# Performance work log

Measured on AMD Instinct MI355X. Metric: run time of the kernel, lower is better.

Reference implementation:

```python
import jax, jax.numpy as jnp
import numpy as np

D_MODEL = 1024
D_HEAD = 128


def setup_inputs() -> dict:
    key = jax.random.key(0)
    kx, kq, kk, kv, ko = jax.random.split(key, 5)
    x = jax.random.normal(kx, (4, 2048, D_MODEL), dtype=jnp.float32)
    # xavier-uniform-ish init scale
    s_in = (6.0 / (D_MODEL + D_HEAD)) ** 0.5
    wq = jax.random.uniform(kq, (D_MODEL, D_HEAD), minval=-s_in, maxval=s_in, dtype=jnp.float32)
    wk = jax.random.uniform(kk, (D_MODEL, D_HEAD), minval=-s_in, maxval=s_in, dtype=jnp.float32)
    wv = jax.random.uniform(kv, (D_MODEL, D_HEAD), minval=-s_in, maxval=s_in, dtype=jnp.float32)
    wo = jax.random.uniform(ko, (D_HEAD, D_MODEL), minval=-s_in, maxval=s_in, dtype=jnp.float32)
    return {"x": x, "wq": wq, "wk": wk, "wv": wv, "wo": wo}


def reference(x, wq, wk, wv, wo):
    # x: [b, s, d_model]
    s = x.shape[1]
    scale = 1.0 / (D_HEAD ** 0.5)
    q = jnp.einsum('bsd,dh->bsh', x, wq)
    k = jnp.einsum('bsd,dh->bsh', x, wk)
    v = jnp.einsum('bsd,dh->bsh', x, wv)
    scores = jnp.einsum('bqh,bkh->bqk', q, k) * scale  # [b, s, s]
    causal = jnp.tril(jnp.ones((s, s), dtype=bool))
    scores = jnp.where(causal, scores, -jnp.inf)
    attn = jax.nn.softmax(scores, axis=-1)
    ctx = jnp.einsum('bqk,bkh->bqh', attn, v)
    return jnp.einsum('bsh,hd->bsd', ctx, wo)
```

## Files before the change

### kernel.cpp

```cpp
#include <hip/hip_runtime.h>
#include <hip/hip_bf16.h>
#include <math.h>

typedef _Float16 half8 __attribute__((ext_vector_type(8)));
typedef _Float16 half4_t __attribute__((ext_vector_type(4)));
typedef _Float16 half2_t __attribute__((ext_vector_type(2)));
typedef float floatx4 __attribute__((ext_vector_type(4)));
typedef float floatx2 __attribute__((ext_vector_type(2)));

#define MFMA16(a, b, c) __builtin_amdgcn_mfma_f32_16x16x32_f16(a, b, c, 0, 0, 0)
#define MASKVAL (-30000.0f)
#define QSCALE 0.1275261529f

__global__ __launch_bounds__(256) void wprep(
    const float* __restrict__ wq, const float* __restrict__ wk,
    const float* __restrict__ wv, const float* __restrict__ wo,
    _Float16* __restrict__ wqt, _Float16* __restrict__ wkt,
    _Float16* __restrict__ wvt, _Float16* __restrict__ wot) {
  __shared__ float T[32][36];
  int bx = blockIdx.x, tid = threadIdx.x;
  const float* src;
  _Float16* dst;
  int R, C, r0, c0;
  float sc = 1.0f;
  if (bx < 384) {
    int p = bx >> 7, t = bx & 127;
    src = (p == 0) ? wq : (p == 1) ? wk : wv;
    dst = (p == 0) ? wqt : (p == 1) ? wkt : wvt;
    if (p == 0) sc = QSCALE;
    R = 1024; C = 128;
    r0 = (t & 31) * 32; c0 = (t >> 5) * 32;
  } else {
    int t = bx - 384;
    src = wo; dst = wot;
    R = 128; C = 1024;
    r0 = (t & 3) * 32; c0 = (t >> 2) * 32;
  }
  {
    int row = tid >> 3, c4 = (tid & 7) * 4;
    float4 f = *(const float4*)&src[(size_t)(r0 + row) * C + c0 + c4];
    T[row][c4] = f.x; T[row][c4 + 1] = f.y; T[row][c4 + 2] = f.z; T[row][c4 + 3] = f.w;
  }
  __syncthreads();
  {
    int cc = tid >> 3, r4 = (tid & 7) * 4;
    half4_t h;
    h[0] = (_Float16)(T[r4 + 0][cc] * sc);
    h[1] = (_Float16)(T[r4 + 1][cc] * sc);
    h[2] = (_Float16)(T[r4 + 2][cc] * sc);
    h[3] = (_Float16)(T[r4 + 3][cc] * sc);
    *(half4_t*)&dst[(size_t)(c0 + cc) * R + r0 + r4] = h;
  }
}

__global__ __launch_bounds__(256, 3) void qkv_gemm(
    const float* __restrict__ x, const _Float16* __restrict__ wqt,
    const _Float16* __restrict__ wkt, const _Float16* __restrict__ wvt,
    _Float16* __restrict__ Qh, _Float16* __restrict__ Kh,
    _Float16* __restrict__ Vt) {
  __shared__ _Float16 A_lds[32 * 136];
  __shared__ _Float16 B_lds[128 * 136];
  int tid = threadIdx.x;
  int w = tid >> 6, lane = tid & 63, quad = lane >> 4, l16 = lane & 15;
  int m0 = blockIdx.x * 32;
  int proj = blockIdx.y;
  const _Float16* wt = (proj == 0) ? wqt : (proj == 1) ? wkt : wvt;
  floatx4 zero = {0.f, 0.f, 0.f, 0.f};
  floatx4 acc[4];
#pragma unroll
  for (int t = 0; t < 4; t++) acc[t] = zero;

  int arow = tid >> 3, ac0 = (tid & 7) * 16;
  int brow = tid >> 1, bc0 = (tid & 1) * 64;
  int mw = (w >> 1) * 16, nw = (w & 1) * 64;

  const float* asrc = x + (size_t)(m0 + arow) * 1024 + ac0;
  const _Float16* bsrc = wt + (size_t)brow * 1024 + bc0;

  float4 af[4];
  half8 bf[8];
#pragma unroll
  for (int i = 0; i < 4; i++) af[i] = ((const float4*)asrc)[i];
#pragma unroll
  for (int i = 0; i < 8; i++) bf[i] = ((const half8*)bsrc)[i];

  for (int k0 = 0; k0 < 1024; k0 += 128) {
    {
      half8 h0, h1;
      h0[0] = (_Float16)af[0].x; h0[1] = (_Float16)af[0].y;
      h0[2] = (_Float16)af[0].z; h0[3] = (_Float16)af[0].w;
      h0[4] = (_Float16)af[1].x; h0[5] = (_Float16)af[1].y;
      h0[6] = (_Float16)af[1].z; h0[7] = (_Float16)af[1].w;
      h1[0] = (_Float16)af[2].x; h1[1] = (_Float16)af[2].y;
      h1[2] = (_Float16)af[2].z; h1[3] = (_Float16)af[2].w;
      h1[4] = (_Float16)af[3].x; h1[5] = (_Float16)af[3].y;
      h1[6] = (_Float16)af[3].z; h1[7] = (_Float16)af[3].w;
      *(half8*)&A_lds[arow * 136 + ac0] = h0;
      *(half8*)&A_lds[arow * 136 + ac0 + 8] = h1;
    }
#pragma unroll
    for (int i = 0; i < 8; i++)
      *(half8*)&B_lds[brow * 136 + bc0 + i * 8] = bf[i];
    __syncthreads();

    if (k0 + 128 < 1024) {
      const float* a2 = asrc + k0 + 128;
      const _Float16* b2 = bsrc + k0 + 128;
#pragma unroll
      for (int i = 0; i < 4; i++) af[i] = ((const float4*)a2)[i];
#pragma unroll
      for (int i = 0; i < 8; i++) bf[i] = ((const half8*)b2)[i];
    }

    half8 a[4];
#pragma unroll
    for (int c = 0; c < 4; c++)
      a[c] = *(const half8*)&A_lds[(mw + l16) * 136 + c * 32 + quad * 8];
#pragma unroll
    for (int t = 0; t < 4; t++)
#pragma unroll
      for (int c = 0; c < 4; c++) {
        half8 b = *(const half8*)&B_lds[(nw + t * 16 + l16) * 136 + c * 32 + quad * 8];
        acc[t] = MFMA16(a[c], b, acc[t]);
      }
    __syncthreads();
  }
#pragma unroll
  for (int t = 0; t < 4; t++)
#pragma unroll
    for (int r = 0; r < 4; r++) {
      int row = m0 + mw + quad * 4 + r;
      int col = nw + t * 16 + l16;
      _Float16 v = (_Float16)acc[t][r];
      if (proj == 0)
        Qh[(size_t)row * 128 + col] = v;
      else if (proj == 1)
        Kh[(size_t)row * 128 + col] = v;
      else {
        int bb = row >> 11, s = row & 2047;
        Vt[((size_t)(bb * 128 + col)) * 2048 + s] = v;
      }
    }
}

__global__ __launch_bounds__(256, 3) void attn_partial(
    const _Float16* __restrict__ Qh, const _Float16* __restrict__ Kh,
    const _Float16* __restrict__ Vt, _Float16* __restrict__ Opart,
    float* __restrict__ Ml) {
  __shared__ _Float16 KV_lds[128 * 136];
  __shared__ _Float16 P_lds[4 * 16 * 136];
  int tid = threadIdx.x;
  int w = tid >> 6, lane = tid & 63, quad = lane >> 4, l16 = lane & 15;
  int g = (int)blockIdx.x;
  int b = g & 3;
  int r = 271 - (g >> 2);
  int m = (int)sqrtf((float)r + 1.0f);
  while (m * (m + 1) > r) m--;
  while ((m + 1) * (m + 2) <= r) m++;
  int s1 = (m + 1) * (m + 1);
  int qt, kc;
  if (r >= s1) { qt = 2 * m + 1; kc = r - s1; }
  else         { qt = 2 * m;     kc = r - m * (m + 1); }
  int q0 = qt * 64, k0 = kc * 128;
  int qw0 = q0 + w * 16;
  int sidx = (b * 32 + qt) * 16 + kc;

  const _Float16* Kb = Kh + (size_t)b * 2048 * 128;
  const _Float16* Vb = Vt + (size_t)b * 128 * 2048;

  int srow = tid >> 1, scol = (tid & 1) * 64;
#pragma unroll
  for (int i = 0; i < 8; i++)
    *(half8*)&KV_lds[srow * 136 + scol + i * 8] =
        *(const half8*)&Kb[(size_t)(k0 + srow) * 128 + scol + i * 8];
  half8 vreg[8];
#pragma unroll
  for (int i = 0; i < 8; i++)
    vreg[i] = *(const half8*)&Vb[(size_t)srow * 2048 + k0 + scol + i * 8];

  half8 aq[4];
  {
    const _Float16* qbase = Qh + (size_t)(b * 2048 + qw0 + l16) * 128;
#pragma unroll
    for (int c = 0; c < 4; c++) aq[c] = *(const half8*)&qbase[c * 32 + quad * 8];
  }
  __syncthreads();

  floatx4 zero = {0.f, 0.f, 0.f, 0.f};
  floatx4 sa[8];
#pragma unroll
  for (int t = 0; t < 8; t++) sa[t] = zero;
#pragma unroll
  for (int t = 0; t < 8; t++)
#pragma unroll
    for (int c = 0; c < 4; c++) {
      half8 bk = *(const half8*)&KV_lds[(t * 16 + l16) * 136 + c * 32 + quad * 8];
      sa[t] = MFMA16(aq[c], bk, sa[t]);
    }

  float m_r[4], l_r[4];
#pragma unroll
  for (int r2 = 0; r2 < 4; r2++) {
    int query = qw0 + quad * 4 + r2;
    float mx = MASKVAL;
#pragma unroll
    for (int t = 0; t < 8; t++) {
      float s = (k0 + t * 16 + l16 > query) ? MASKVAL : sa[t][r2];
      sa[t][r2] = s;
      mx = fmaxf(mx, s);
    }
#pragma unroll
    for (int off = 1; off < 16; off <<= 1) mx = fmaxf(mx, __shfl_xor(mx, off));
    float rs = 0.f;
#pragma unroll
    for (int t = 0; t < 8; t++) {
      float e = exp2f(sa[t][r2] - mx);
      sa[t][r2] = e;
      rs += e;
    }
#pragma unroll
    for (int off = 1; off < 16; off <<= 1) rs += __shfl_xor(rs, off);
    m_r[r2] = mx;
    l_r[r2] = rs;
  }

  __syncthreads();

#pragma unroll
  for (int i = 0; i < 8; i++)
    *(half8*)&KV_lds[srow * 136 + scol + i * 8] = vreg[i];
  _Float16* P = P_lds + w * 16 * 136;
#pragma unroll
  for (int r2 = 0; r2 < 4; r2++)
#pragma unroll
    for (int t = 0; t < 8; t++)
      P[(quad * 4 + r2) * 136 + t * 16 + l16] = (_Float16)sa[t][r2];
  __syncthreads();

  floatx4 O[8];
#pragma unroll
  for (int t = 0; t < 8; t++) O[t] = zero;
#pragma unroll
  for (int c2 = 0; c2 < 4; c2++) {
    half8 ap = *(const half8*)&P[l16 * 136 + c2 * 32 + quad * 8];
#pragma unroll
    for (int t = 0; t < 8; t++) {
      half8 bv = *(const half8*)&KV_lds[(t * 16 + l16) * 136 + c2 * 32 + quad * 8];
      O[t] = MFMA16(ap, bv, O[t]);
    }
  }

  size_t obase = (size_t)sidx * 8192;
#pragma unroll
  for (int t = 0; t < 8; t++)
#pragma unroll
    for (int r2 = 0; r2 < 4; r2++)
      Opart[obase + (size_t)(w * 16 + quad * 4 + r2) * 128 + t * 16 + l16] = (_Float16)O[t][r2];
  if (l16 == 0)
#pragma unroll
    for (int r2 = 0; r2 < 4; r2++) {
      int row = w * 16 + quad * 4 + r2;
      floatx2 ml;
      ml[0] = m_r[r2];
      ml[1] = l_r[r2];
      *(floatx2*)&Ml[(size_t)sidx * 128 + row * 2] = ml;
    }
}

__global__ __launch_bounds__(256) void attn_combine(
    const _Float16* __restrict__ Opart, const float* __restrict__ Ml,
    _Float16* __restrict__ ctx) {
  int tid = threadIdx.x;
  int w = tid >> 6, lane = tid & 63;
  int row = blockIdx.x * 4 + w;
  int b = row >> 11, s = row & 2047;
  int qt = s >> 6, ri = s & 63;
  int nkc = (qt + 2) >> 1;
  int sidx0 = (b * 32 + qt) * 16;
  float M = MASKVAL;
  for (int i = 0; i < nkc; i++)
    M = fmaxf(M, Ml[(size_t)(sidx0 + i) * 128 + ri * 2]);
  float L = 0.f, a0 = 0.f, a1 = 0.f;
  for (int i = 0; i < nkc; i++) {
    float mi = Ml[(size_t)(sidx0 + i) * 128 + ri * 2];
    float li = Ml[(size_t)(sidx0 + i) * 128 + ri * 2 + 1];
    float sc = exp2f(mi - M);
    L += li * sc;
    half2_t o = *(const half2_t*)&Opart[(size_t)(sidx0 + i) * 8192 + (size_t)ri * 128 + lane * 2];
    a0 += sc * (float)o[0];
    a1 += sc * (float)o[1];
  }
  float inv = 1.f / L;
  half2_t hv;
  hv[0] = (_Float16)(a0 * inv);
  hv[1] = (_Float16)(a1 * inv);
  *(half2_t*)&ctx[(size_t)row * 128 + lane * 2] = hv;
}

__global__ __launch_bounds__(256) void out_gemm(
    const _Float16* __restrict__ ctx, const _Float16* __restrict__ wot,
    float* __restrict__ out) {
  __shared__ _Float16 A_lds[64 * 136];
  __shared__ _Float16 B_lds[128 * 136];
  int tid = threadIdx.x;
  int w = tid >> 6, lane = tid & 63, quad = lane >> 4, l16 = lane & 15;
  int m0 = blockIdx.x * 64, n0 = blockIdx.y * 128;
  {
    int row = tid >> 2, kk = (tid & 3) * 32;
#pragma unroll
    for (int i = 0; i < 4; i++)
      *(half8*)&A_lds[row * 136 + kk + i * 8] =
          *(const half8*)&ctx[(size_t)(m0 + row) * 128 + kk + i * 8];
  }
  {
    int n = tid >> 1, kk = (tid & 1) * 64;
#pragma unroll
    for (int i = 0; i < 8; i++)
      *(half8*)&B_lds[n * 136 + kk + i * 8] =
          *(const half8*)&wot[(size_t)(n0 + n) * 128 + kk + i * 8];
  }
  __syncthreads();
  floatx4 zero = {0.f, 0.f, 0.f, 0.f};
  floatx4 acc[8];
#pragma unroll
  for (int t = 0; t < 8; t++) acc[t] = zero;
  half8 a[4];
#pragma unroll
  for (int c = 0; c < 4; c++) a[c] = *(const half8*)&A_lds[(w * 16 + l16) * 136 + c * 32 + quad * 8];
#pragma unroll
  for (int t = 0; t < 8; t++)
#pragma unroll
    for (int c = 0; c < 4; c++) {
      half8 b = *(const half8*)&B_lds[(t * 16 + l16) * 136 + c * 32 + quad * 8];
      acc[t] = MFMA16(a[c], b, acc[t]);
    }
#pragma unroll
  for (int t = 0; t < 8; t++)
#pragma unroll
    for (int r = 0; r < 4; r++) {
      int row = m0 + w * 16 + quad * 4 + r;
      out[(size_t)row * 1024 + n0 + t * 16 + l16] = acc[t][r];
    }
}

extern "C" void kernel_launch(void* const* d_in, const int* in_sizes, int n_in,
                              void* d_out, int out_size, void* d_ws, size_t ws_size,
                              hipStream_t stream) {
  const float* x = (const float*)d_in[0];
  const float* wq = (const float*)d_in[1];
  const float* wk = (const float*)d_in[2];
  const float* wv = (const float*)d_in[3];
  const float* wo = (const float*)d_in[4];
  char* ws = (char*)d_ws;
  _Float16* wqt = (_Float16*)(ws + 0);
  _Float16* wkt = (_Float16*)(ws + 262144);
  _Float16* wvt = (_Float16*)(ws + 524288);
  _Float16* wot = (_Float16*)(ws + 786432);
  _Float16* Qh  = (_Float16*)(ws + 1048576);
  _Float16* Kh  = (_Float16*)(ws + 3145728);
  _Float16* Vt  = (_Float16*)(ws + 5242880);
  _Float16* ctxh = (_Float16*)(ws + 7340032);
  _Float16* Opart = (_Float16*)(ws + 9437184);
  float* Ml = (float*)(ws + 42991616);
  float* out = (float*)d_out;

  wprep<<<512, 256, 0, stream>>>(wq, wk, wv, wo, wqt, wkt, wvt, wot);
  qkv_gemm<<<dim3(256, 3), 256, 0, stream>>>(x, wqt, wkt, wvt, Qh, Kh, Vt);
  attn_partial<<<1088, 256, 0, stream>>>(Qh, Kh, Vt, Opart, Ml);
  attn_combine<<<2048, 256, 0, stream>>>(Opart, Ml, ctxh);
  out_gemm<<<dim3(128, 8), 256, 0, stream>>>(ctxh, wot, out);
}
```

Measured before the change: 161.2 us.

## Split attention KV into 256-wide chunks with online softmax; coalesce V transpose store

```diff
diff --git a/kernel.cpp b/kernel.cpp
--- a/kernel.cpp
+++ b/kernel.cpp
@@ -125,22 +125,36 @@
       }
     __syncthreads();
   }
-#pragma unroll
-  for (int t = 0; t < 4; t++)
-#pragma unroll
-    for (int r = 0; r < 4; r++) {
-      int row = m0 + mw + quad * 4 + r;
-      int col = nw + t * 16 + l16;
-      _Float16 v = (_Float16)acc[t][r];
-      if (proj == 0)
-        Qh[(size_t)row * 128 + col] = v;
-      else if (proj == 1)
-        Kh[(size_t)row * 128 + col] = v;
-      else {
-        int bb = row >> 11, s = row & 2047;
-        Vt[((size_t)(bb * 128 + col)) * 2048 + s] = v;
-      }
-    }
+  if (proj < 2) {
+#pragma unroll
+    for (int t = 0; t < 4; t++)
+#pragma unroll
+      for (int r = 0; r < 4; r++) {
+        int row = m0 + mw + quad * 4 + r;
+        int col = nw + t * 16 + l16;
+        _Float16 v = (_Float16)acc[t][r];
+        if (proj == 0) Qh[(size_t)row * 128 + col] = v;
+        else           Kh[(size_t)row * 128 + col] = v;
+      }
+  } else {
+    _Float16* Vl = B_lds;
+#pragma unroll
+    for (int t = 0; t < 4; t++)
+#pragma unroll
+      for (int r = 0; r < 4; r++) {
+        int lrow = mw + quad * 4 + r;
+        int col = nw + t * 16 + l16;
+        Vl[col * 40 + lrow] = (_Float16)acc[t][r];
+      }
+    __syncthreads();
+    int col = tid >> 1, hh = tid & 1;
+    int bb = m0 >> 11, s0 = (m0 & 2047) + hh * 16;
+    half8 h0 = *(half8*)&Vl[col * 40 + hh * 16];
+    half8 h1 = *(half8*)&Vl[col * 40 + hh * 16 + 8];
+    _Float16* dstv = Vt + ((size_t)(bb * 128 + col)) * 2048 + s0;
+    *(half8*)&dstv[0] = h0;
+    *(half8*)&dstv[8] = h1;
+  }
 }
 
 __global__ __launch_bounds__(256, 3) void attn_partial(
@@ -153,30 +167,24 @@
   int w = tid >> 6, lane = tid & 63, quad = lane >> 4, l16 = lane & 15;
   int g = (int)blockIdx.x;
   int b = g & 3;
-  int r = 271 - (g >> 2);
-  int m = (int)sqrtf((float)r + 1.0f);
-  while (m * (m + 1) > r) m--;
-  while ((m + 1) * (m + 2) <= r) m++;
-  int s1 = (m + 1) * (m + 1);
-  int qt, kc;
-  if (r >= s1) { qt = 2 * m + 1; kc = r - s1; }
-  else         { qt = 2 * m;     kc = r - m * (m + 1); }
-  int q0 = qt * 64, k0 = kc * 128;
+  int r = g >> 2;
+  int m = (int)sqrtf((float)r * 0.5f);
+  while (2 * m * (m + 1) > r) m--;
+  while (2 * (m + 1) * (m + 2) <= r) m++;
+  int r0_ = r - 2 * m * (m + 1);
+  int qdiv = r0_ / (m + 1);
+  int qt = 4 * m + qdiv;
+  int kc = r0_ - qdiv * (m + 1);
+  int q0 = qt * 64, k0 = kc * 256;
+  int kmax = (qt + 1) * 64;
+  int len = kmax - k0; if (len > 256) len = 256;
+  int nsub = (len + 127) >> 7;
   int qw0 = q0 + w * 16;
-  int sidx = (b * 32 + qt) * 16 + kc;
-
-  const _Float16* Kb = Kh + (size_t)b * 2048 * 128;
+  int sidx = (b * 32 + qt) * 8 + kc;
+
+  const _Float16* Kb = Qh;
+  Kb = Kh + (size_t)b * 2048 * 128;
   const _Float16* Vb = Vt + (size_t)b * 128 * 2048;
-
-  int srow = tid >> 1, scol = (tid & 1) * 64;
-#pragma unroll
-  for (int i = 0; i < 8; i++)
-    *(half8*)&KV_lds[srow * 136 + scol + i * 8] =
-        *(const half8*)&Kb[(size_t)(k0 + srow) * 128 + scol + i * 8];
-  half8 vreg[8];
-#pragma unroll
-  for (int i = 0; i < 8; i++)
-    vreg[i] = *(const half8*)&Vb[(size_t)srow * 2048 + k0 + scol + i * 8];
 
   half8 aq[4];
   {
@@ -184,85 +192,108 @@
 #pragma unroll
     for (int c = 0; c < 4; c++) aq[c] = *(const half8*)&qbase[c * 32 + quad * 8];
   }
-  __syncthreads();
-
+
+  int srow = tid >> 1, scol = (tid & 1) * 64;
   floatx4 zero = {0.f, 0.f, 0.f, 0.f};
-  floatx4 sa[8];
-#pragma unroll
-  for (int t = 0; t < 8; t++) sa[t] = zero;
+  floatx4 O[8];
+#pragma unroll
+  for (int t = 0; t < 8; t++) O[t] = zero;
+  float m_r[4] = {MASKVAL, MASKVAL, MASKVAL, MASKVAL};
+  float l_r[4] = {0.f, 0.f, 0.f, 0.f};
+
+  for (int s = 0; s < nsub; s++) {
+    int ks = k0 + s * 128;
+    if (s) __syncthreads();
+#pragma unroll
+    for (int i = 0; i < 8; i++)
+      *(half8*)&KV_lds[srow * 136 + scol + i * 8] =
+          *(const half8*)&Kb[(size_t)(ks + srow) * 128 + scol + i * 8];
+    half8 vreg[8];
+#pragma unroll
+    for (int i = 0; i < 8; i++)
+      vreg[i] = *(const half8*)&Vb[(size_t)srow * 2048 + ks + scol + i * 8];
+    __syncthreads();
+
+    floatx4 sa[8];
+#pragma unroll
+    for (int t = 0; t < 8; t++) sa[t] = zero;
+#pragma unroll
+    for (int t = 0; t < 8; t++)
+#pragma unroll
+      for (int c = 0; c < 4; c++) {
+        half8 bk = *(const half8*)&KV_lds[(t * 16 + l16) * 136 + c * 32 + quad * 8];
+        sa[t] = MFMA16(aq[c], bk, sa[t]);
+      }
+
+    float sc[4];
+#pragma unroll
+    for (int j = 0; j < 4; j++) {
+      int query = qw0 + quad * 4 + j;
+      float mx = MASKVAL;
+#pragma unroll
+      for (int t = 0; t < 8; t++) {
+        float v = (ks + t * 16 + l16 > query) ? MASKVAL : sa[t][j];
+        sa[t][j] = v;
+        mx = fmaxf(mx, v);
+      }
+#pragma unroll
+      for (int off = 1; off < 16; off <<= 1) mx = fmaxf(mx, __shfl_xor(mx, off));
+      float mnew = fmaxf(m_r[j], mx);
+      float scj = exp2f(m_r[j] - mnew);
+      float rs = 0.f;
+#pragma unroll
+      for (int t = 0; t < 8; t++) {
+        float e = exp2f(sa[t][j] - mnew);
+        sa[t][j] = e;
+        rs += e;
+      }
+#pragma unroll
+      for (int off = 1; off < 16; off <<= 1) rs += __shfl_xor(rs, off);
+      l_r[j] = l_r[j] * scj + rs;
+      m_r[j] = mnew;
+      sc[j] = scj;
+    }
+#pragma unroll
+    for (int t = 0; t < 8; t++)
+#pragma unroll
+      for (int j = 0; j < 4; j++) O[t][j] *= sc[j];
+
+    __syncthreads();
+#pragma unroll
+    for (int i = 0; i < 8; i++)
+      *(half8*)&KV_lds[srow * 136 + scol + i * 8] = vreg[i];
+    _Float16* P = P_lds + w * 16 * 136;
+#pragma unroll
+    for (int j = 0; j < 4; j++)
+#pragma unroll
+      for (int t = 0; t < 8; t++)
+        P[(quad * 4 + j) * 136 + t * 16 + l16] = (_Float16)sa[t][j];
+    __syncthreads();
+
+#pragma unroll
+    for (int c2 = 0; c2 < 4; c2++) {
+      half8 ap = *(const half8*)&P[l16 * 136 + c2 * 32 + quad * 8];
+#pragma unroll
+      for (int t = 0; t < 8; t++) {
+        half8 bv = *(const half8*)&KV_lds[(t * 16 + l16) * 136 + c2 * 32 + quad * 8];
+        O[t] = MFMA16(ap, bv, O[t]);
+      }
+    }
+  }
+
+  size_t obase = (size_t)sidx * 8192;
 #pragma unroll
   for (int t = 0; t < 8; t++)
 #pragma unroll
-    for (int c = 0; c < 4; c++) {
-      half8 bk = *(const half8*)&KV_lds[(t * 16 + l16) * 136 + c * 32 + quad * 8];
-      sa[t] = MFMA16(aq[c], bk, sa[t]);
-    }
-
-  float m_r[4], l_r[4];
-#pragma unroll
-  for (int r2 = 0; r2 < 4; r2++) {
-    int query = qw0 + quad * 4 + r2;
-    float mx = MASKVAL;
-#pragma unroll
-    for (int t = 0; t < 8; t++) {
-      float s = (k0 + t * 16 + l16 > query) ? MASKVAL : sa[t][r2];
-      sa[t][r2] = s;
-      mx = fmaxf(mx, s);
-    }
-#pragma unroll
-    for (int off = 1; off < 16; off <<= 1) mx = fmaxf(mx, __shfl_xor(mx, off));
-    float rs = 0.f;
-#pragma unroll
-    for (int t = 0; t < 8; t++) {
-      float e = exp2f(sa[t][r2] - mx);
-      sa[t][r2] = e;
-      rs += e;
-    }
-#pragma unroll
-    for (int off = 1; off < 16; off <<= 1) rs += __shfl_xor(rs, off);
-    m_r[r2] = mx;
-    l_r[r2] = rs;
-  }
-
-  __syncthreads();
-
-#pragma unroll
-  for (int i = 0; i < 8; i++)
-    *(half8*)&KV_lds[srow * 136 + scol + i * 8] = vreg[i];
-  _Float16* P = P_lds + w * 16 * 136;
-#pragma unroll
-  for (int r2 = 0; r2 < 4; r2++)
-#pragma unroll
-    for (int t = 0; t < 8; t++)
-      P[(quad * 4 + r2) * 136 + t * 16 + l16] = (_Float16)sa[t][r2];
-  __syncthreads();
-
-  floatx4 O[8];
-#pragma unroll
-  for (int t = 0; t < 8; t++) O[t] = zero;
-#pragma unroll
-  for (int c2 = 0; c2 < 4; c2++) {
-    half8 ap = *(const half8*)&P[l16 * 136 + c2 * 32 + quad * 8];
-#pragma unroll
-    for (int t = 0; t < 8; t++) {
-      half8 bv = *(const half8*)&KV_lds[(t * 16 + l16) * 136 + c2 * 32 + quad * 8];
-      O[t] = MFMA16(ap, bv, O[t]);
-    }
-  }
-
-  size_t obase = (size_t)sidx * 8192;
-#pragma unroll
-  for (int t = 0; t < 8; t++)
-#pragma unroll
-    for (int r2 = 0; r2 < 4; r2++)
-      Opart[obase + (size_t)(w * 16 + quad * 4 + r2) * 128 + t * 16 + l16] = (_Float16)O[t][r2];
+    for (int j = 0; j < 4; j++)
+      Opart[obase + (size_t)(w * 16 + quad * 4 + j) * 128 + t * 16 + l16] = (_Float16)O[t][j];
   if (l16 == 0)
 #pragma unroll
-    for (int r2 = 0; r2 < 4; r2++) {
-      int row = w * 16 + quad * 4 + r2;
+    for (int j = 0; j < 4; j++) {
+      int row = w * 16 + quad * 4 + j;
       floatx2 ml;
-      ml[0] = m_r[r2];
-      ml[1] = l_r[r2];
+      ml[0] = m_r[j];
+      ml[1] = l_r[j];
       *(floatx2*)&Ml[(size_t)sidx * 128 + row * 2] = ml;
     }
 }
@@ -275,20 +306,29 @@
   int row = blockIdx.x * 4 + w;
   int b = row >> 11, s = row & 2047;
   int qt = s >> 6, ri = s & 63;
-  int nkc = (qt + 2) >> 1;
-  int sidx0 = (b * 32 + qt) * 16;
+  int nkc = (qt + 4) >> 2;
+  int sidx0 = (b * 32 + qt) * 8;
+  float mv[8], lv[8];
+#pragma unroll
+  for (int i = 0; i < 8; i++) {
+    if (i < nkc) {
+      floatx2 ml = *(const floatx2*)&Ml[(size_t)(sidx0 + i) * 128 + ri * 2];
+      mv[i] = ml[0]; lv[i] = ml[1];
+    } else { mv[i] = MASKVAL; lv[i] = 0.f; }
+  }
   float M = MASKVAL;
-  for (int i = 0; i < nkc; i++)
-    M = fmaxf(M, Ml[(size_t)(sidx0 + i) * 128 + ri * 2]);
+#pragma unroll
+  for (int i = 0; i < 8; i++) M = fmaxf(M, mv[i]);
   float L = 0.f, a0 = 0.f, a1 = 0.f;
-  for (int i = 0; i < nkc; i++) {
-    float mi = Ml[(size_t)(sidx0 + i) * 128 + ri * 2];
-    float li = Ml[(size_t)(sidx0 + i) * 128 + ri * 2 + 1];
-    float sc = exp2f(mi - M);
-    L += li * sc;
-    half2_t o = *(const half2_t*)&Opart[(size_t)(sidx0 + i) * 8192 + (size_t)ri * 128 + lane * 2];
-    a0 += sc * (float)o[0];
-    a1 += sc * (float)o[1];
+#pragma unroll
+  for (int i = 0; i < 8; i++) {
+    if (i < nkc) {
+      float scv = exp2f(mv[i] - M);
+      L += lv[i] * scv;
+      half2_t o = *(const half2_t*)&Opart[(size_t)(sidx0 + i) * 8192 + (size_t)ri * 128 + lane * 2];
+      a0 += scv * (float)o[0];
+      a1 += scv * (float)o[1];
+    }
   }
   float inv = 1.f / L;
   half2_t hv;
@@ -361,12 +401,12 @@
   _Float16* Vt  = (_Float16*)(ws + 5242880);
   _Float16* ctxh = (_Float16*)(ws + 7340032);
   _Float16* Opart = (_Float16*)(ws + 9437184);
-  float* Ml = (float*)(ws + 42991616);
+  float* Ml = (float*)(ws + 26214400);
   float* out = (float*)d_out;
 
   wprep<<<512, 256, 0, stream>>>(wq, wk, wv, wo, wqt, wkt, wvt, wot);
   qkv_gemm<<<dim3(256, 3), 256, 0, stream>>>(x, wqt, wkt, wvt, Qh, Kh, Vt);
-  attn_partial<<<1088, 256, 0, stream>>>(Qh, Kh, Vt, Opart, Ml);
+  attn_partial<<<576, 256, 0, stream>>>(Qh, Kh, Vt, Opart, Ml);
   attn_combine<<<2048, 256, 0, stream>>>(Opart, Ml, ctxh);
   out_gemm<<<dim3(128, 8), 256, 0, stream>>>(ctxh, wot, out);
 }
```

New measurement: 156.8 us. -2.7%, faster.
